# Kernel optimization log

Measured on AMD Instinct MI355X. Metric: run time of the kernel, lower is better.

Reference implementation:

```python
import jax, jax.numpy as jnp
import numpy as np

B, N, DIM, H, DH = 2, 2048, 1024, 16, 64
SCALE = 8.0
LN_EPS = 1e-5
L2_EPS = 1e-12


def setup_inputs() -> dict:
    key = jax.random.key(0)
    ks = jax.random.split(key, 6)
    s = 0.02  # keep projections at sane magnitude
    return {
        "x": jax.random.normal(ks[0], (B, N, DIM), dtype=jnp.float32),
        "g": jnp.ones((DIM,), dtype=jnp.float32),
        "b": jnp.zeros((DIM,), dtype=jnp.float32),
        "c_attn_w": jax.random.normal(ks[1], (DIM, 3 * DIM), dtype=jnp.float32) * s,
        "c_attn_b": jax.random.normal(ks[2], (3 * DIM,), dtype=jnp.float32) * s,
        "c_proj_w": jax.random.normal(ks[3], (DIM, DIM), dtype=jnp.float32) * s,
        "c_proj_b": jax.random.normal(ks[4], (DIM,), dtype=jnp.float32) * s,
        "to_out_w": jax.random.normal(ks[5], (DIM, DIM), dtype=jnp.float32) * s,
    }


def _l2norm(t):
    # F.normalize(t, dim=-1): t / max(||t||, eps)
    n = jnp.sqrt(jnp.sum(t * t, axis=-1, keepdims=True))
    return t / jnp.maximum(n, L2_EPS)


def reference(x, g, b, c_attn_w, c_attn_b, c_proj_w, c_proj_b, to_out_w):
    # LayerNorm
    mu = jnp.mean(x, axis=-1, keepdims=True)
    var = jnp.mean(jnp.square(x - mu), axis=-1, keepdims=True)
    y = (x - mu) * jax.lax.rsqrt(var + LN_EPS) * g + b  # [B,N,DIM]

    # GPT2 Conv1D c_attn: y @ W + b, split into q/k/v
    qkv = y @ c_attn_w + c_attn_b  # [B,N,3*DIM]
    q, k, v = jnp.split(qkv, 3, axis=-1)

    def split_heads(t):
        return t.reshape(B, N, H, DH).transpose(0, 2, 1, 3)  # [B,H,N,DH]

    q, k, v = split_heads(q), split_heads(k), split_heads(v)

    # cosine-sim attention: L2-normalize q,k, scaled dot product, causal softmax
    qn, kn = _l2norm(q), _l2norm(k)
    sim = jnp.einsum("bhid,bhjd->bhij", qn, kn) * SCALE  # [B,H,N,N]
    mask_value = -jnp.finfo(sim.dtype).max
    causal = jnp.triu(jnp.ones((N, N), dtype=bool), k=1)
    sim = jnp.where(causal, mask_value, sim)
    attn = jax.nn.softmax(sim, axis=-1)
    o = jnp.einsum("bhij,bhjd->bhid", attn, v)  # [B,H,N,DH]

    o = o.transpose(0, 2, 1, 3).reshape(B, N, DIM)
    o = o @ c_proj_w + c_proj_b          # Conv1D c_proj
    out = o @ to_out_w.T                  # Linear to_out (no bias)
    return out
```

## Files before the change

### kernel.cpp

```cpp
#include <hip/hip_runtime.h>
#include <cstdint>
#include <cstddef>

#define Bb 2
#define Nn 2048
#define DIMM 1024
#define Hh 16
#define DHh 64
#define BH (Bb*Hh)
#define MROWS (Bb*Nn)

typedef __bf16 bf16x8 __attribute__((ext_vector_type(8)));
typedef float f32x4 __attribute__((ext_vector_type(4)));
typedef short s16x4 __attribute__((ext_vector_type(4)));

__device__ __forceinline__ unsigned short f2bf(float f) {
  unsigned u = __float_as_uint(f);
  u += 0x7FFFu + ((u >> 16) & 1u);
  return (unsigned short)(u >> 16);
}
__device__ __forceinline__ unsigned short f2bf_fast(float f) {
  return (unsigned short)((__float_as_uint(f) + 0x8000u) >> 16);
}
__device__ __forceinline__ float bf2f(unsigned short s) {
  return __uint_as_float(((unsigned)s) << 16);
}

#define GLDS16(g, l) __builtin_amdgcn_global_load_lds( \
    (const __attribute__((address_space(1))) void*)(g), \
    (__attribute__((address_space(3))) void*)(l), 16, 0, 0)

__global__ __launch_bounds__(256) void prep_kernel(
    const float* __restrict__ x, const float* __restrict__ g,
    const float* __restrict__ b,
    const float* __restrict__ c_attn_w, const float* __restrict__ c_proj_w,
    const float* __restrict__ to_out_w, const float* __restrict__ c_proj_b,
    unsigned short* __restrict__ y,
    unsigned short* __restrict__ wqkv, unsigned short* __restrict__ wpbf,
    unsigned short* __restrict__ wout, float* __restrict__ bc) {
  int bid = blockIdx.x;
  int t = threadIdx.x;
  if (bid < 4096) {
    int row = bid;
    const float4* xr = (const float4*)(x + (size_t)row * DIMM);
    float4 v = xr[t];
    float s  = v.x + v.y + v.z + v.w;
    float ss = v.x*v.x + v.y*v.y + v.z*v.z + v.w*v.w;
    #pragma unroll
    for (int o = 1; o < 64; o <<= 1) { s += __shfl_xor(s, o); ss += __shfl_xor(ss, o); }
    __shared__ float red[8];
    int wv = t >> 6;
    if ((t & 63) == 0) { red[wv] = s; red[wv + 4] = ss; }
    __syncthreads();
    s  = red[0] + red[1] + red[2] + red[3];
    ss = red[4] + red[5] + red[6] + red[7];
    float mu  = s * (1.0f / DIMM);
    float var = ss * (1.0f / DIMM) - mu * mu;
    float rs  = rsqrtf(var + 1e-5f);
    float4 gv = ((const float4*)g)[t];
    float4 bv = ((const float4*)b)[t];
    ushort4 o4;
    o4.x = f2bf((v.x - mu) * rs * gv.x + bv.x);
    o4.y = f2bf((v.y - mu) * rs * gv.y + bv.y);
    o4.z = f2bf((v.z - mu) * rs * gv.z + bv.z);
    o4.w = f2bf((v.w - mu) * rs * gv.w + bv.w);
    ((ushort4*)y)[(size_t)row * 256 + t] = o4;
  } else if (bid < 7168) {
    __shared__ float tile[32][33];
    int bb = bid - 4096;
    int bx = bb % 96, by = bb / 96;
    int tx = t & 31, ty = t >> 5;
    int x2 = bx * 32 + tx;
    int y0 = by * 32;
    #pragma unroll
    for (int j = 0; j < 32; j += 8)
      tile[ty + j][tx] = c_attn_w[(size_t)(y0 + ty + j) * 3072 + x2];
    __syncthreads();
    int ox  = by * 32 + tx;
    int oy0 = bx * 32;
    #pragma unroll
    for (int j = 0; j < 32; j += 8)
      wqkv[(size_t)(oy0 + ty + j) * 1024 + ox] = f2bf(tile[tx][ty + j]);
  } else if (bid < 9216) {
    bool iswp = bid < 8192;
    int bb = bid - (iswp ? 7168 : 8192);
    const float* in = iswp ? c_proj_w : to_out_w;
    unsigned short* out = iswp ? wpbf : wout;
    int i = (bb * 256 + t) * 4;
    float4 v = *(const float4*)(in + i);
    ushort4 o;
    o.x = f2bf(v.x); o.y = f2bf(v.y); o.z = f2bf(v.z); o.w = f2bf(v.w);
    *(ushort4*)(out + i) = o;
  } else {
    int n = (bid - 9216) * 4 + (t >> 6);
    int lane = t & 63;
    const float4* w = (const float4*)(to_out_w + (size_t)n * DIMM);
    const float4* b4 = (const float4*)c_proj_b;
    float s = 0.0f;
    #pragma unroll
    for (int k = 0; k < 4; k++) {
      float4 wv = w[lane + k * 64], bv = b4[lane + k * 64];
      s += wv.x * bv.x + wv.y * bv.y + wv.z * bv.z + wv.w * bv.w;
    }
    #pragma unroll
    for (int o = 1; o < 64; o <<= 1) s += __shfl_xor(s, o);
    if (lane == 0) bc[n] = s;
  }
}

template <int EPI>
__device__ __forceinline__ void gemm_body(
    const unsigned short* __restrict__ A, const unsigned short* __restrict__ Bt,
    const float* __restrict__ bias,
    unsigned short* __restrict__ obf, float* __restrict__ of32,
    unsigned short* __restrict__ q_std, unsigned short* __restrict__ k_std,
    unsigned short* __restrict__ vt_out,
    int M, int N, int K, int bn, int bm,
    unsigned short* smem) {
  int t = threadIdx.x;
  int lane = t & 63, wv = t >> 6;
  int wm = (wv >> 1) * 32, wn = (wv & 1) * 64;
  int l16 = lane & 15, quad = lane >> 4;

  const unsigned short* Ab = A + (size_t)(bm * 128) * K;
  const unsigned short* Bb2 = Bt + (size_t)(bn * 128) * K;
  int srow = t >> 3;
  int gch = (t & 7) ^ (srow & 7);

  f32x4 acc[2][4] = {};
  const int KT = K >> 6;

  auto stage = [&](int kt_, int b_) {
    unsigned short* dA = smem + b_ * 16384;
    unsigned short* dB = dA + 8192;
    const unsigned short* gA = Ab  + (size_t)srow * K + kt_ * 64 + gch * 8;
    const unsigned short* gB = Bb2 + (size_t)srow * K + kt_ * 64 + gch * 8;
    #pragma unroll
    for (int i = 0; i < 2; i++) {
      GLDS16(gA + (size_t)(64 * i) * K, dA + (size_t)(t + 512 * i) * 8);
      GLDS16(gB + (size_t)(64 * i) * K, dB + (size_t)(t + 512 * i) * 8);
    }
  };

  stage(0, 0);
  if (KT > 1) stage(1, 1);

  for (int kt2 = 0; kt2 < KT; ++kt2) {
    if (kt2 < KT - 1) asm volatile("s_waitcnt vmcnt(4)" ::: "memory");
    else              asm volatile("s_waitcnt vmcnt(0)" ::: "memory");
    __builtin_amdgcn_s_barrier();
    __builtin_amdgcn_sched_barrier(0);
    const unsigned short* sA = smem + (kt2 & 1) * 16384;
    const unsigned short* sB = sA + 8192;
    #pragma unroll
    for (int kk = 0; kk < 2; kk++) {
      int slot = (kk * 4 + quad) ^ (l16 & 7);
      bf16x8 af[2], bfr[4];
      #pragma unroll
      for (int i = 0; i < 2; i++)
        af[i] = *(const bf16x8*)(sA + (size_t)(wm + i * 16 + l16) * 64 + slot * 8);
      #pragma unroll
      for (int j = 0; j < 4; j++)
        bfr[j] = *(const bf16x8*)(sB + (size_t)(wn + j * 16 + l16) * 64 + slot * 8);
      __builtin_amdgcn_s_setprio(1);
      #pragma unroll
      for (int i = 0; i < 2; i++)
        #pragma unroll
        for (int j = 0; j < 4; j++)
          acc[i][j] = __builtin_amdgcn_mfma_f32_16x16x32_bf16(af[i], bfr[j], acc[i][j], 0, 0, 0);
      __builtin_amdgcn_s_setprio(0);
    }
    __builtin_amdgcn_sched_barrier(0);
    __builtin_amdgcn_s_barrier();
    __builtin_amdgcn_sched_barrier(0);
    if (kt2 + 2 < KT) stage(kt2 + 2, kt2 & 1);
  }

  float bvals[4];
  #pragma unroll
  for (int j = 0; j < 4; j++)
    bvals[j] = (EPI == 3) ? 0.0f : bias[bn * 128 + wn + j * 16 + l16];

  if (EPI == 0) {
    int which = bn >> 3;
    if (which < 2) {
      #pragma unroll
      for (int i = 0; i < 2; i++) {
        #pragma unroll
        for (int r = 0; r < 4; r++) {
          int m = bm * 128 + wm + i * 16 + quad * 4 + r;
          float vals[4];
          float ss = 0.0f;
          #pragma unroll
          for (int j = 0; j < 4; j++) {
            vals[j] = acc[i][j][r] + bvals[j];
            ss += vals[j] * vals[j];
          }
          ss += __shfl_xor(ss, 1); ss += __shfl_xor(ss, 2);
          ss += __shfl_xor(ss, 4); ss += __shfl_xor(ss, 8);
          float scale = ((which == 0) ? 8.0f : 1.0f) / fmaxf(sqrtf(ss), 1e-12f);
          int bi = m >> 11, ns = m & 2047;
          unsigned short* dst = (which == 0) ? q_std : k_std;
          #pragma unroll
          for (int j = 0; j < 4; j++) {
            int n = bn * 128 + wn + j * 16 + l16;
            int nn2 = n & 1023;
            int h = nn2 >> 6, d = nn2 & 63;
            dst[((size_t)((bi * Hh + h) * Nn + ns)) * DHh + d] = f2bf(vals[j] * scale);
          }
        }
      }
    } else {
      __syncthreads();
      #pragma unroll
      for (int i = 0; i < 2; i++) {
        int mchunk = (wm + i * 16) / 4 + quad;
        #pragma unroll
        for (int j = 0; j < 4; j++) {
          int n_local = wn + j * 16 + l16;
          int sw = mchunk ^ (n_local & 31);
          ushort4 pack;
          pack.x = f2bf(acc[i][j][0] + bvals[j]);
          pack.y = f2bf(acc[i][j][1] + bvals[j]);
          pack.z = f2bf(acc[i][j][2] + bvals[j]);
          pack.w = f2bf(acc[i][j][3] + bvals[j]);
          *(ushort4*)(smem + (size_t)n_local * 128 + sw * 4) = pack;
        }
      }
      __syncthreads();
      int drow = t >> 2, mq = t & 3;
      int h = (bn - 16) * 2 + (drow >> 6);
      int d = drow & 63;
      int bi = bm >> 4;
      int ns0 = (bm * 128) & 2047;
      unsigned short* dst = vt_out + ((size_t)(bi * Hh + h) * DHh + d) * Nn + ns0 + mq * 32;
      #pragma unroll
      for (int cc = 0; cc < 8; cc++) {
        int c0 = mq * 8 + cc;
        int s0 = c0 ^ (drow & 31);
        *(ushort4*)(dst + cc * 4) = *(const ushort4*)(smem + (size_t)drow * 128 + s0 * 4);
      }
    }
  } else {
    #pragma unroll
    for (int i = 0; i < 2; i++) {
      #pragma unroll
      for (int j = 0; j < 4; j++) {
        int n = bn * 128 + wn + j * 16 + l16;
        #pragma unroll
        for (int r = 0; r < 4; r++) {
          int m = bm * 128 + wm + i * 16 + quad * 4 + r;
          float val = acc[i][j][r] + bvals[j];
          if (EPI == 2) of32[(size_t)m * N + n] = val;
          else          obf[(size_t)m * N + n] = f2bf(val);
        }
      }
    }
  }
}

__global__ __launch_bounds__(512, 4) void gemm_qkv_wcomb(
    const unsigned short* __restrict__ y, const unsigned short* __restrict__ wqkv,
    const float* __restrict__ c_attn_b,
    unsigned short* __restrict__ q_std, unsigned short* __restrict__ k_std,
    unsigned short* __restrict__ vt_out,
    const unsigned short* __restrict__ wout, const unsigned short* __restrict__ wpbf,
    unsigned short* __restrict__ wcomb) {
  __shared__ unsigned short smem[32768];
  int bn = blockIdx.x, bm = blockIdx.y;
  if (bn < 24) {
    gemm_body<0>(y, wqkv, c_attn_b, nullptr, nullptr, q_std, k_std, vt_out,
                 MROWS, 3 * DIMM, DIMM, bn, bm, smem);
  } else {
    int idx = (bn - 24) * 32 + bm;
    gemm_body<3>(wout, wpbf, nullptr, wcomb, nullptr, nullptr, nullptr, nullptr,
                 DIMM, DIMM, DIMM, idx & 7, idx >> 3, smem);
  }
}

__global__ __launch_bounds__(512, 4) void gemm_final(
    const unsigned short* __restrict__ A, const unsigned short* __restrict__ Bt,
    const float* __restrict__ bias, float* __restrict__ of32) {
  __shared__ unsigned short smem[32768];
  gemm_body<2>(A, Bt, bias, nullptr, of32, nullptr, nullptr, nullptr,
               MROWS, DIMM, DIMM, blockIdx.x, blockIdx.y, smem);
}

__global__ __launch_bounds__(512, 4) void attn_kernel(
    const unsigned short* __restrict__ qn, const unsigned short* __restrict__ kn,
    const unsigned short* __restrict__ vt, unsigned short* __restrict__ o_flat) {
  __shared__ float smemf[8704];
  int t = threadIdx.x, lane = t & 63, wv = t >> 6;
  int half = wv >> 2, strip = wv & 3;
  int l16 = lane & 15, quad = lane >> 4;
  int id = blockIdx.x;
  int qb = (id < 256) ? (15 - (id >> 5)) : ((id - 256) >> 5);
  int bh = id & 31;
  int m0 = qb * 128 + strip * 32;
  const unsigned short* qbase = qn + (size_t)bh * Nn * DHh;
  const unsigned short* kbase = kn + (size_t)bh * Nn * DHh;
  const unsigned short* vbase = vt + (size_t)bh * DHh * Nn;

  unsigned short* myK = (unsigned short*)((char*)smemf + half * 16384);
  unsigned short* myV = (unsigned short*)((char*)smemf + half * 16384 + 8192);

  bf16x8 aq[2][2];
  #pragma unroll
  for (int i2 = 0; i2 < 2; i2++)
    #pragma unroll
    for (int kk = 0; kk < 2; kk++)
      aq[i2][kk] = *(const bf16x8*)(qbase + (size_t)(m0 + i2 * 16 + l16) * DHh + kk * 32 + quad * 8);

  f32x4 accOT[4][2] = {};
  float den[2] = {};

  int tl = t & 255;
  int srow = tl >> 3;
  int gch = (tl & 7) ^ (srow & 7);
  int nh = qb + 1;
  int kt0 = half * nh;

  for (int kt = 0; kt < nh; kt++) {
    int j0 = (kt0 + kt) * 64;
    __syncthreads();
    GLDS16(kbase + (size_t)(j0 + srow)      * DHh + gch * 8, myK + (size_t)tl * 8);
    GLDS16(kbase + (size_t)(j0 + srow + 32) * DHh + gch * 8, myK + (size_t)(tl + 256) * 8);
    GLDS16(vbase + (size_t)srow        * Nn + j0 + gch * 8, myV + (size_t)tl * 8);
    GLDS16(vbase + (size_t)(srow + 32) * Nn + j0 + gch * 8, myV + (size_t)(tl + 256) * 8);
    __syncthreads();

    if (j0 > m0 + 31) continue;

    f32x4 sc[4][2] = {};
    #pragma unroll
    for (int kk = 0; kk < 2; kk++) {
      int slot = (kk * 4 + quad) ^ (l16 & 7);
      #pragma unroll
      for (int jt = 0; jt < 4; jt++) {
        bf16x8 ak = *(const bf16x8*)(myK + (size_t)(jt * 16 + l16) * 64 + slot * 8);
        #pragma unroll
        for (int i2 = 0; i2 < 2; i2++)
          sc[jt][i2] = __builtin_amdgcn_mfma_f32_16x16x32_bf16(ak, aq[i2][kk], sc[jt][i2], 0, 0, 0);
      }
    }

    bool fullTile = (j0 + 63) <= m0;
    s16x4 pf[4][2];
    #pragma unroll
    for (int jt = 0; jt < 4; jt++) {
      #pragma unroll
      for (int i2 = 0; i2 < 2; i2++) {
        int m = m0 + i2 * 16 + l16;
        #pragma unroll
        for (int r = 0; r < 4; r++) {
          int j = j0 + jt * 16 + quad * 4 + r;
          float p;
          if (fullTile) p = __expf(sc[jt][i2][r] - 8.0f);
          else          p = (j <= m) ? __expf(sc[jt][i2][r] - 8.0f) : 0.0f;
          den[i2] += p;
          pf[jt][i2][r] = (short)f2bf_fast(p);
        }
      }
    }

    #pragma unroll
    for (int jt = 0; jt < 4; jt++) {
      #pragma unroll
      for (int dt = 0; dt < 4; dt++) {
        int row = dt * 16 + l16;
        int ch = (jt * 2 + (quad >> 1)) ^ (l16 & 7);
        s16x4 av = *(const s16x4*)(myV + (size_t)row * 64 + ch * 8 + (quad & 1) * 4);
        #pragma unroll
        for (int i2 = 0; i2 < 2; i2++)
          accOT[dt][i2] = __builtin_amdgcn_mfma_f32_16x16x16bf16_1k(av, pf[jt][i2], accOT[dt][i2], 0, 0, 0);
      }
    }
  }

  #pragma unroll
  for (int i2 = 0; i2 < 2; i2++) {
    float d = den[i2];
    d += __shfl_xor(d, 16); d += __shfl_xor(d, 32);
    den[i2] = d;
  }

  __syncthreads();
  float* scr = smemf + strip * 2176;
  if (half == 1) {
    #pragma unroll
    for (int dt = 0; dt < 4; dt++)
      #pragma unroll
      for (int i2 = 0; i2 < 2; i2++)
        *(f32x4*)(scr + ((size_t)(dt * 2 + i2) * 64 + lane) * 4) = accOT[dt][i2];
    scr[2048 + lane] = den[0];
    scr[2048 + 64 + lane] = den[1];
  }
  __syncthreads();
  if (half == 0) {
    float dinv[2];
    dinv[0] = 1.0f / (den[0] + scr[2048 + lane]);
    dinv[1] = 1.0f / (den[1] + scr[2048 + 64 + lane]);
    int bi = bh >> 4, h = bh & 15;
    #pragma unroll
    for (int i2 = 0; i2 < 2; i2++) {
      #pragma unroll
      for (int dt = 0; dt < 4; dt++) {
        f32x4 o = accOT[dt][i2] + *(const f32x4*)(scr + ((size_t)(dt * 2 + i2) * 64 + lane) * 4);
        ushort4 o4;
        o4.x = f2bf(o[0] * dinv[i2]);
        o4.y = f2bf(o[1] * dinv[i2]);
        o4.z = f2bf(o[2] * dinv[i2]);
        o4.w = f2bf(o[3] * dinv[i2]);
        int ns = m0 + i2 * 16 + l16;
        int d0 = dt * 16 + quad * 4;
        *(ushort4*)(o_flat + ((size_t)(bi * Nn + ns)) * DIMM + h * DHh + d0) = o4;
      }
    }
  }
}

extern "C" void kernel_launch(void* const* d_in, const int* in_sizes, int n_in,
                              void* d_out, int out_size, void* d_ws, size_t ws_size,
                              hipStream_t stream) {
  const float* x        = (const float*)d_in[0];
  const float* g        = (const float*)d_in[1];
  const float* b        = (const float*)d_in[2];
  const float* c_attn_w = (const float*)d_in[3];
  const float* c_attn_b = (const float*)d_in[4];
  const float* c_proj_w = (const float*)d_in[5];
  const float* c_proj_b = (const float*)d_in[6];
  const float* to_out_w = (const float*)d_in[7];
  float* out = (float*)d_out;

  char* p = (char*)d_ws;
  unsigned short* y     = (unsigned short*)(p + ((size_t)0  << 20));
  unsigned short* qbuf  = (unsigned short*)(p + ((size_t)8  << 20));
  unsigned short* kbuf  = (unsigned short*)(p + ((size_t)16 << 20));
  unsigned short* vtb   = (unsigned short*)(p + ((size_t)24 << 20));
  unsigned short* wpbf  = (unsigned short*)(p + ((size_t)32 << 20));
  unsigned short* wout  = (unsigned short*)(p + ((size_t)34 << 20));
  unsigned short* wqkv  = (unsigned short*)(p + ((size_t)40 << 20));
  unsigned short* wcomb = (unsigned short*)(p + ((size_t)46 << 20));
  float*          bc    = (float*)        (p + ((size_t)48 << 20));

  prep_kernel<<<9472, 256, 0, stream>>>(x, g, b, c_attn_w, c_proj_w, to_out_w,
                                        c_proj_b, y, wqkv, wpbf, wout, bc);
  gemm_qkv_wcomb<<<dim3(26, MROWS / 128), 512, 0, stream>>>(
      y, wqkv, c_attn_b, qbuf, kbuf, vtb, wout, wpbf, wcomb);
  attn_kernel<<<512, 512, 0, stream>>>(qbuf, kbuf, vtb, y);
  gemm_final<<<dim3(DIMM / 128, MROWS / 128), 512, 0, stream>>>(y, wcomb, bc, out);
}
```

Before: 193.5 us.

## Double-buffer K/V tiles in attention with async prefetch and MFMA priority

The attention kernel now keeps two K/V shared-memory buffers per half and prefetches tile kt+2 while computing tile kt. Waits on vmcnt replace the full syncthreads around each load. It also raises wave priority around the MFMA sections. Shared memory per block roughly doubles to 64KB, which may cut occupancy from the requested 4 blocks per CU.

```diff
diff --git a/kernel.cpp b/kernel.cpp
--- a/kernel.cpp
+++ b/kernel.cpp
@@ -289,7 +289,7 @@
 __global__ __launch_bounds__(512, 4) void attn_kernel(
     const unsigned short* __restrict__ qn, const unsigned short* __restrict__ kn,
     const unsigned short* __restrict__ vt, unsigned short* __restrict__ o_flat) {
-  __shared__ float smemf[8704];
+  __shared__ float smemf[16384];
   int t = threadIdx.x, lane = t & 63, wv = t >> 6;
   int half = wv >> 2, strip = wv & 3;
   int l16 = lane & 15, quad = lane >> 4;
@@ -301,9 +301,6 @@
   const unsigned short* kbase = kn + (size_t)bh * Nn * DHh;
   const unsigned short* vbase = vt + (size_t)bh * DHh * Nn;
 
-  unsigned short* myK = (unsigned short*)((char*)smemf + half * 16384);
-  unsigned short* myV = (unsigned short*)((char*)smemf + half * 16384 + 8192);
-
   bf16x8 aq[2][2];
   #pragma unroll
   for (int i2 = 0; i2 < 2; i2++)
@@ -320,61 +317,83 @@
   int nh = qb + 1;
   int kt0 = half * nh;
 
+  auto stageT = [&](int kt_, int b_) {
+    int jj = (kt0 + kt_) * 64;
+    unsigned short* K_ = (unsigned short*)((char*)smemf + half * 32768 + b_ * 16384);
+    unsigned short* V_ = K_ + 4096;
+    GLDS16(kbase + (size_t)(jj + srow)      * DHh + gch * 8, K_ + (size_t)tl * 8);
+    GLDS16(kbase + (size_t)(jj + srow + 32) * DHh + gch * 8, K_ + (size_t)(tl + 256) * 8);
+    GLDS16(vbase + (size_t)srow        * Nn + jj + gch * 8, V_ + (size_t)tl * 8);
+    GLDS16(vbase + (size_t)(srow + 32) * Nn + jj + gch * 8, V_ + (size_t)(tl + 256) * 8);
+  };
+
+  stageT(0, 0);
+  if (nh > 1) stageT(1, 1);
+
   for (int kt = 0; kt < nh; kt++) {
+    if (kt < nh - 1) asm volatile("s_waitcnt vmcnt(4)" ::: "memory");
+    else             asm volatile("s_waitcnt vmcnt(0)" ::: "memory");
+    __builtin_amdgcn_s_barrier();
+    __builtin_amdgcn_sched_barrier(0);
     int j0 = (kt0 + kt) * 64;
-    __syncthreads();
-    GLDS16(kbase + (size_t)(j0 + srow)      * DHh + gch * 8, myK + (size_t)tl * 8);
-    GLDS16(kbase + (size_t)(j0 + srow + 32) * DHh + gch * 8, myK + (size_t)(tl + 256) * 8);
-    GLDS16(vbase + (size_t)srow        * Nn + j0 + gch * 8, myV + (size_t)tl * 8);
-    GLDS16(vbase + (size_t)(srow + 32) * Nn + j0 + gch * 8, myV + (size_t)(tl + 256) * 8);
-    __syncthreads();
-
-    if (j0 > m0 + 31) continue;
-
-    f32x4 sc[4][2] = {};
-    #pragma unroll
-    for (int kk = 0; kk < 2; kk++) {
-      int slot = (kk * 4 + quad) ^ (l16 & 7);
+    unsigned short* myK = (unsigned short*)((char*)smemf + half * 32768 + (kt & 1) * 16384);
+    unsigned short* myV = myK + 4096;
+
+    if (j0 <= m0 + 31) {
+      f32x4 sc[4][2] = {};
+      #pragma unroll
+      for (int kk = 0; kk < 2; kk++) {
+        int slot = (kk * 4 + quad) ^ (l16 & 7);
+        __builtin_amdgcn_s_setprio(1);
+        #pragma unroll
+        for (int jt = 0; jt < 4; jt++) {
+          bf16x8 ak = *(const bf16x8*)(myK + (size_t)(jt * 16 + l16) * 64 + slot * 8);
+          #pragma unroll
+          for (int i2 = 0; i2 < 2; i2++)
+            sc[jt][i2] = __builtin_amdgcn_mfma_f32_16x16x32_bf16(ak, aq[i2][kk], sc[jt][i2], 0, 0, 0);
+        }
+        __builtin_amdgcn_s_setprio(0);
+      }
+
+      bool fullTile = (j0 + 63) <= m0;
+      s16x4 pf[4][2];
       #pragma unroll
       for (int jt = 0; jt < 4; jt++) {
-        bf16x8 ak = *(const bf16x8*)(myK + (size_t)(jt * 16 + l16) * 64 + slot * 8);
-        #pragma unroll
-        for (int i2 = 0; i2 < 2; i2++)
-          sc[jt][i2] = __builtin_amdgcn_mfma_f32_16x16x32_bf16(ak, aq[i2][kk], sc[jt][i2], 0, 0, 0);
-      }
-    }
-
-    bool fullTile = (j0 + 63) <= m0;
-    s16x4 pf[4][2];
-    #pragma unroll
-    for (int jt = 0; jt < 4; jt++) {
-      #pragma unroll
-      for (int i2 = 0; i2 < 2; i2++) {
-        int m = m0 + i2 * 16 + l16;
-        #pragma unroll
-        for (int r = 0; r < 4; r++) {
-          int j = j0 + jt * 16 + quad * 4 + r;
-          float p;
-          if (fullTile) p = __expf(sc[jt][i2][r] - 8.0f);
-          else          p = (j <= m) ? __expf(sc[jt][i2][r] - 8.0f) : 0.0f;
-          den[i2] += p;
-          pf[jt][i2][r] = (short)f2bf_fast(p);
-        }
-      }
-    }
-
-    #pragma unroll
-    for (int jt = 0; jt < 4; jt++) {
-      #pragma unroll
-      for (int dt = 0; dt < 4; dt++) {
-        int row = dt * 16 + l16;
-        int ch = (jt * 2 + (quad >> 1)) ^ (l16 & 7);
-        s16x4 av = *(const s16x4*)(myV + (size_t)row * 64 + ch * 8 + (quad & 1) * 4);
-        #pragma unroll
-        for (int i2 = 0; i2 < 2; i2++)
-          accOT[dt][i2] = __builtin_amdgcn_mfma_f32_16x16x16bf16_1k(av, pf[jt][i2], accOT[dt][i2], 0, 0, 0);
-      }
-    }
+        #pragma unroll
+        for (int i2 = 0; i2 < 2; i2++) {
+          int m = m0 + i2 * 16 + l16;
+          #pragma unroll
+          for (int r = 0; r < 4; r++) {
+            int j = j0 + jt * 16 + quad * 4 + r;
+            float p;
+            if (fullTile) p = __expf(sc[jt][i2][r] - 8.0f);
+            else          p = (j <= m) ? __expf(sc[jt][i2][r] - 8.0f) : 0.0f;
+            den[i2] += p;
+            pf[jt][i2][r] = (short)f2bf_fast(p);
+          }
+        }
+      }
+
+      #pragma unroll
+      for (int jt = 0; jt < 4; jt++) {
+        __builtin_amdgcn_s_setprio(1);
+        #pragma unroll
+        for (int dt = 0; dt < 4; dt++) {
+          int row = dt * 16 + l16;
+          int ch = (jt * 2 + (quad >> 1)) ^ (l16 & 7);
+          s16x4 av = *(const s16x4*)(myV + (size_t)row * 64 + ch * 8 + (quad & 1) * 4);
+          #pragma unroll
+          for (int i2 = 0; i2 < 2; i2++)
+            accOT[dt][i2] = __builtin_amdgcn_mfma_f32_16x16x16bf16_1k(av, pf[jt][i2], accOT[dt][i2], 0, 0, 0);
+        }
+        __builtin_amdgcn_s_setprio(0);
+      }
+    }
+
+    __builtin_amdgcn_sched_barrier(0);
+    __builtin_amdgcn_s_barrier();
+    __builtin_amdgcn_sched_barrier(0);
+    if (kt + 2 < nh) stageT(kt + 2, kt & 1);
   }
 
   #pragma unroll
```

Result: no change. 190.8 us (-1.4%).
